# Kernel tuning notes

Hardware: AMD Instinct MI355X
Metric: run time of the kernel (lower is better)

## Reference

```python
import jax, jax.numpy as jnp
import numpy as np

NUM_NODES = 50000

def _gat_conv(x, edge_index, W, a_src, a_dst, b):
    # PyG GATConv, heads=1: h = x W ; e_ij = LeakyReLU(a_src.h_j + a_dst.h_i)
    # softmax over incoming edges of i ; out_i = sum_j alpha_ij h_j + b
    h = x @ W                                  # [N, F]
    src, dst = edge_index[0], edge_index[1]    # edge j->i : src=j, dst=i
    alpha_s = h @ a_src                        # [N]
    alpha_d = h @ a_dst                        # [N]
    e = jax.nn.leaky_relu(alpha_s[src] + alpha_d[dst], negative_slope=0.2)  # [E]
    # segment softmax over destination nodes
    e_max = jax.ops.segment_max(e, dst, num_segments=NUM_NODES)
    e_exp = jnp.exp(e - e_max[dst])
    denom = jax.ops.segment_sum(e_exp, dst, num_segments=NUM_NODES)
    coef = e_exp / denom[dst]                  # [E]
    out = jax.ops.segment_sum(h[src] * coef[:, None], dst, num_segments=NUM_NODES)
    return out + b

def setup_inputs() -> dict:
    key = jax.random.key(0)
    ks = jax.random.split(key, 10)
    N, E, IN, HID, OUT = NUM_NODES, 800000, 256, 256, 128
    x = jax.random.normal(ks[0], (N, IN), dtype=jnp.float32)
    edge_index = jax.random.randint(ks[1], (2, E), 0, N, dtype=jnp.int32)
    def glorot(k, shape):
        lim = float(np.sqrt(6.0 / (shape[0] + shape[-1])))
        return jax.random.uniform(k, shape, jnp.float32, -lim, lim)
    return {
        'x': x,
        'edge_index': edge_index,
        'W1': glorot(ks[2], (IN, HID)),
        'a_src1': glorot(ks[3], (HID,)),
        'a_dst1': glorot(ks[4], (HID,)),
        'b1': jnp.zeros((HID,), jnp.float32),
        'W2': glorot(ks[5], (HID, OUT)),
        'a_src2': glorot(ks[6], (OUT,)),
        'a_dst2': glorot(ks[7], (OUT,)),
        'b2': jnp.zeros((OUT,), jnp.float32),
    }

def reference(x, edge_index, W1, a_src1, a_dst1, b1, W2, a_src2, a_dst2, b2):
    # add self loops once (same edge_index used by both convs)
    ar = jnp.arange(NUM_NODES, dtype=edge_index.dtype)
    ei = jnp.concatenate([edge_index, jnp.stack([ar, ar])], axis=1)
    x1 = _gat_conv(x, ei, W1, a_src1, a_dst1, b1)
    h = jax.nn.relu(x1)          # dropout p=0.3 is identity in eval mode
    x2 = _gat_conv(h, ei, W2, a_src2, a_dst2, b2)
    return (x2, h)
```

## Files before the change

kernel.cpp:

```cpp
#include <hip/hip_runtime.h>
#include <hip/hip_bf16.h>

#define N_NODES 50000
#define E0      800000
#define ETOT    850000

typedef __bf16 bf16x8 __attribute__((ext_vector_type(8)));
typedef float  f32x4  __attribute__((ext_vector_type(4)));
typedef ushort u16x8  __attribute__((ext_vector_type(8)));
union B8 { u16x8 u; bf16x8 b; };

static __device__ __forceinline__ float b2f(ushort u) {
    union { uint u; float f; } x; x.u = ((uint)u) << 16; return x.f;
}
static __device__ __forceinline__ ushort f2bf(float f) {
    uint u = __builtin_bit_cast(uint, f);
    uint r = (u + 0x7FFFu + ((u >> 16) & 1u)) >> 16;
    return (ushort)r;
}


__global__ __launch_bounds__(256) void k_deg(const int* __restrict__ ei, int* __restrict__ deg) {
    int e = blockIdx.x * 256 + threadIdx.x;
    if (e >= ETOT) return;
    int dst = (e < E0) ? ei[E0 + e] : (e - E0);
    atomicAdd(&deg[dst], 1);
}

__global__ __launch_bounds__(256) void k_scan1(const int* __restrict__ deg, int* __restrict__ offs,
                                               int* __restrict__ bsum) {
    __shared__ int buf[256];
    int tid = threadIdx.x;
    int i = blockIdx.x * 256 + tid;
    int v = (i < N_NODES) ? deg[i] : 0;
    buf[tid] = v;
    __syncthreads();
    for (int off = 1; off < 256; off <<= 1) {
        int t = (tid >= off) ? buf[tid - off] : 0;
        __syncthreads();
        buf[tid] += t;
        __syncthreads();
    }
    if (i < N_NODES) offs[i + 1] = buf[tid];
    if (tid == 255) bsum[blockIdx.x] = buf[255];
}

__global__ __launch_bounds__(256) void k_scan2(int* __restrict__ bsum, int nb) {
    __shared__ int buf[256];
    int tid = threadIdx.x;
    int v = (tid < nb) ? bsum[tid] : 0;
    buf[tid] = v;
    __syncthreads();
    for (int off = 1; off < 256; off <<= 1) {
        int t = (tid >= off) ? buf[tid - off] : 0;
        __syncthreads();
        buf[tid] += t;
        __syncthreads();
    }
    if (tid < nb) bsum[tid] = buf[tid] - v;
}

__global__ __launch_bounds__(256) void k_scan3(int* __restrict__ offs, const int* __restrict__ bsum) {
    int tid = threadIdx.x;
    int i = blockIdx.x * 256 + tid;
    if (i < N_NODES) offs[i + 1] += bsum[blockIdx.x];
    if (i == 0) offs[0] = 0;
}

__global__ __launch_bounds__(256) void k_copy(const int* __restrict__ offs, int* __restrict__ cursor) {
    int i = blockIdx.x * 256 + threadIdx.x;
    if (i < N_NODES) cursor[i] = offs[i];
}

__global__ __launch_bounds__(256) void k_scatter(const int* __restrict__ ei, int* __restrict__ cursor,
                                                 int* __restrict__ esrc) {
    int e = blockIdx.x * 256 + threadIdx.x;
    if (e >= ETOT) return;
    int src, dst;
    if (e < E0) { src = ei[e]; dst = ei[E0 + e]; }
    else        { src = e - E0; dst = src; }
    int pos = atomicAdd(&cursor[dst], 1);
    esrc[pos] = src;
}

__global__ __launch_bounds__(256) void k_splitT(const float* __restrict__ W, ushort* __restrict__ th,
                                                ushort* __restrict__ tl, int K, int N) {
    int i = blockIdx.x * 256 + threadIdx.x;
    if (i >= K * N) return;
    int n = i / K, k = i - n * K;
    float v = W[(size_t)k * N + n];
    ushort h = f2bf(v);
    th[(size_t)n * K + k] = h;
    tl[(size_t)n * K + k] = f2bf(v - b2f(h));
}


static __device__ __forceinline__ void split8r(const float4 r0, const float4 r1, bf16x8& hi, bf16x8& lo) {
    float vv[8] = { r0.x, r0.y, r0.z, r0.w, r1.x, r1.y, r1.z, r1.w };
    B8 H, L;
#pragma unroll
    for (int i = 0; i < 8; ++i) {
        uint u = __builtin_bit_cast(uint, vv[i]);
        H.u[i] = (ushort)(u >> 16);
        float hf = __builtin_bit_cast(float, u & 0xffff0000u);
        L.u[i] = (ushort)(__builtin_bit_cast(uint, vv[i] - hf) >> 16);
    }
    hi = H.b; lo = L.b;
}

__global__ __launch_bounds__(256) void k_gemm_mfma(const float* __restrict__ A,
                                                   const ushort* __restrict__ Bth, const ushort* __restrict__ Btl,
                                                   ushort* __restrict__ Cb, int M, int Nn) {
    constexpr int K = 256;
    int tid = threadIdx.x;
    int wid = tid >> 6, lane = tid & 63;
    int wr = wid >> 1, wc = wid & 1;
    int bm = blockIdx.x * 128, bn = blockIdx.y * 128;
    int lr = lane & 15, lg = lane >> 4;

    f32x4 acc[4][4] = {};

    const float* Ap[4];
#pragma unroll
    for (int m = 0; m < 4; ++m) {
        int row = bm + wr * 64 + m * 16 + lr;
        if (row >= M) row = M - 1;
        Ap[m] = A + (size_t)row * K + lg * 8;
    }
    const ushort* Bhp[4];
    const ushort* Blp[4];
#pragma unroll
    for (int n = 0; n < 4; ++n) {
        int col = bn + wc * 64 + n * 16 + lr;
        Bhp[n] = Bth + (size_t)col * K + lg * 8;
        Blp[n] = Btl + (size_t)col * K + lg * 8;
    }

    float4 aR[2][4][2];
    bf16x8 bH[2][4], bL[2][4];
#pragma unroll
    for (int m = 0; m < 4; ++m) {
        aR[0][m][0] = *(const float4*)(Ap[m]);
        aR[0][m][1] = *(const float4*)(Ap[m] + 4);
    }
#pragma unroll
    for (int n = 0; n < 4; ++n) {
        bH[0][n] = *(const bf16x8*)(Bhp[n]);
        bL[0][n] = *(const bf16x8*)(Blp[n]);
    }

#pragma unroll
    for (int it = 0; it < 8; ++it) {
        const int cur = it & 1, nxt = cur ^ 1;
        if (it < 7) {
            const int kt = (it + 1) * 32;
#pragma unroll
            for (int m = 0; m < 4; ++m) {
                aR[nxt][m][0] = *(const float4*)(Ap[m] + kt);
                aR[nxt][m][1] = *(const float4*)(Ap[m] + kt + 4);
            }
#pragma unroll
            for (int n = 0; n < 4; ++n) {
                bH[nxt][n] = *(const bf16x8*)(Bhp[n] + kt);
                bL[nxt][n] = *(const bf16x8*)(Blp[n] + kt);
            }
        }
        bf16x8 a_h[4], a_l[4];
#pragma unroll
        for (int m = 0; m < 4; ++m) split8r(aR[cur][m][0], aR[cur][m][1], a_h[m], a_l[m]);
#pragma unroll
        for (int m = 0; m < 4; ++m)
#pragma unroll
            for (int n = 0; n < 4; ++n) {
                acc[m][n] = __builtin_amdgcn_mfma_f32_16x16x32_bf16(a_h[m], bH[cur][n], acc[m][n], 0, 0, 0);
                acc[m][n] = __builtin_amdgcn_mfma_f32_16x16x32_bf16(a_l[m], bH[cur][n], acc[m][n], 0, 0, 0);
                acc[m][n] = __builtin_amdgcn_mfma_f32_16x16x32_bf16(a_h[m], bL[cur][n], acc[m][n], 0, 0, 0);
            }
    }
#pragma unroll
    for (int m = 0; m < 4; ++m)
#pragma unroll
        for (int r = 0; r < 4; ++r) {
            int row = bm + wr * 64 + m * 16 + lg * 4 + r;
            if (row < M) {
#pragma unroll
                for (int n = 0; n < 4; ++n) {
                    int col = bn + wc * 64 + n * 16 + lr;
                    Cb[(size_t)row * Nn + col] = f2bf(acc[m][n][r]);
                }
            }
        }
}


template <int F>
__global__ __launch_bounds__(256) void k_alpha(const ushort* __restrict__ H, const float* __restrict__ a_src,
                                               const float* __restrict__ a_dst, float* __restrict__ as,
                                               float* __restrict__ ad) {
    int gw = (blockIdx.x * 256 + threadIdx.x) >> 6;
    int lane = threadIdx.x & 63;
    if (gw >= N_NODES) return;
    float s = 0.f, d = 0.f;
    if (F == 256) {
        ushort4 v = *(const ushort4*)(H + (size_t)gw * 256 + lane * 4);
        float4 cs = *(const float4*)(a_src + lane * 4);
        float4 cd = *(const float4*)(a_dst + lane * 4);
        float f0 = b2f(v.x), f1 = b2f(v.y), f2 = b2f(v.z), f3 = b2f(v.w);
        s = f0 * cs.x + f1 * cs.y + f2 * cs.z + f3 * cs.w;
        d = f0 * cd.x + f1 * cd.y + f2 * cd.z + f3 * cd.w;
    } else {
        ushort2 v = *(const ushort2*)(H + (size_t)gw * 128 + lane * 2);
        float2 cs = *(const float2*)(a_src + lane * 2);
        float2 cd = *(const float2*)(a_dst + lane * 2);
        float f0 = b2f(v.x), f1 = b2f(v.y);
        s = f0 * cs.x + f1 * cs.y;
        d = f0 * cd.x + f1 * cd.y;
    }
    for (int o = 32; o; o >>= 1) { s += __shfl_down(s, o); d += __shfl_down(d, o); }
    if (lane == 0) { as[gw] = s; ad[gw] = d; }
}

template <int F, bool RELU>
__global__ __launch_bounds__(256) void k_aggf(const int* __restrict__ offs, const int* __restrict__ esrc,
                                              const float* __restrict__ as, const float* __restrict__ ad,
                                              const ushort* __restrict__ H, const float* __restrict__ bias,
                                              float* __restrict__ out) {
    constexpr int V = F / 64;
    constexpr float THR = 8.f;
    int gw = (blockIdx.x * 256 + threadIdx.x) >> 6;
    int lane = threadIdx.x & 63;
    if (gw >= N_NODES) return;
    int s0 = offs[gw], s1 = offs[gw + 1];
    float adi = ad[gw];
    float m = -1e30f, ssum = 0.f;
    float acc[V] = {};
    int k = s0;
    for (; k + 3 < s1; k += 4) {
        int r0 = esrc[k], r1 = esrc[k + 1], r2 = esrc[k + 2], r3 = esrc[k + 3];
        float row0[V], row1[V], row2[V], row3[V];
        if (V == 4) {
            ushort4 v0 = *(const ushort4*)(H + (size_t)r0 * F + lane * 4);
            ushort4 v1 = *(const ushort4*)(H + (size_t)r1 * F + lane * 4);
            ushort4 v2 = *(const ushort4*)(H + (size_t)r2 * F + lane * 4);
            ushort4 v3 = *(const ushort4*)(H + (size_t)r3 * F + lane * 4);
            row0[0] = b2f(v0.x); row0[1] = b2f(v0.y); row0[2] = b2f(v0.z); row0[3] = b2f(v0.w);
            row1[0] = b2f(v1.x); row1[1] = b2f(v1.y); row1[2] = b2f(v1.z); row1[3] = b2f(v1.w);
            row2[0] = b2f(v2.x); row2[1] = b2f(v2.y); row2[2] = b2f(v2.z); row2[3] = b2f(v2.w);
            row3[0] = b2f(v3.x); row3[1] = b2f(v3.y); row3[2] = b2f(v3.z); row3[3] = b2f(v3.w);
        } else {
            ushort2 v0 = *(const ushort2*)(H + (size_t)r0 * F + lane * 2);
            ushort2 v1 = *(const ushort2*)(H + (size_t)r1 * F + lane * 2);
            ushort2 v2 = *(const ushort2*)(H + (size_t)r2 * F + lane * 2);
            ushort2 v3 = *(const ushort2*)(H + (size_t)r3 * F + lane * 2);
            row0[0] = b2f(v0.x); row0[1] = b2f(v0.y);
            row1[0] = b2f(v1.x); row1[1] = b2f(v1.y);
            row2[0] = b2f(v2.x); row2[1] = b2f(v2.y);
            row3[0] = b2f(v3.x); row3[1] = b2f(v3.y);
        }
        float e0 = as[r0] + adi; e0 = e0 > 0.f ? e0 : 0.2f * e0;
        float e1 = as[r1] + adi; e1 = e1 > 0.f ? e1 : 0.2f * e1;
        float e2 = as[r2] + adi; e2 = e2 > 0.f ? e2 : 0.2f * e2;
        float e3 = as[r3] + adi; e3 = e3 > 0.f ? e3 : 0.2f * e3;
        float em = fmaxf(fmaxf(e0, e1), fmaxf(e2, e3));
        if (em > m + THR) {
            float sc = __expf(m - em);
            ssum *= sc;
#pragma unroll
            for (int j = 0; j < V; ++j) acc[j] *= sc;
            m = em;
        }
        float w0 = __expf(e0 - m), w1 = __expf(e1 - m);
        float w2 = __expf(e2 - m), w3 = __expf(e3 - m);
        ssum += (w0 + w1) + (w2 + w3);
#pragma unroll
        for (int j = 0; j < V; ++j)
            acc[j] += (w0 * row0[j] + w1 * row1[j]) + (w2 * row2[j] + w3 * row3[j]);
    }
    for (; k < s1; ++k) {
        int r0 = esrc[k];
        float row0[V];
        if (V == 4) {
            ushort4 v0 = *(const ushort4*)(H + (size_t)r0 * F + lane * 4);
            row0[0] = b2f(v0.x); row0[1] = b2f(v0.y); row0[2] = b2f(v0.z); row0[3] = b2f(v0.w);
        } else {
            ushort2 v0 = *(const ushort2*)(H + (size_t)r0 * F + lane * 2);
            row0[0] = b2f(v0.x); row0[1] = b2f(v0.y);
        }
        float e0 = as[r0] + adi; e0 = e0 > 0.f ? e0 : 0.2f * e0;
        if (e0 > m + THR) {
            float sc = __expf(m - e0);
            ssum *= sc;
#pragma unroll
            for (int j = 0; j < V; ++j) acc[j] *= sc;
            m = e0;
        }
        float w0 = __expf(e0 - m);
        ssum += w0;
#pragma unroll
        for (int j = 0; j < V; ++j) acc[j] += w0 * row0[j];
    }
    float inv = 1.f / ssum;
    float r[V];
#pragma unroll
    for (int j = 0; j < V; ++j) {
        r[j] = acc[j] * inv + bias[lane * V + j];
        if (RELU) r[j] = fmaxf(r[j], 0.f);
    }
    if (V == 4) *(float4*)(out + (size_t)gw * F + lane * 4) = make_float4(r[0], r[1], r[2], r[3]);
    else        *(float2*)(out + (size_t)gw * F + lane * 2) = make_float2(r[0], r[1]);
}


static inline size_t al256(size_t x) { return (x + 255) & ~(size_t)255; }

extern "C" void kernel_launch(void* const* d_in, const int* in_sizes, int n_in,
                              void* d_out, int out_size, void* d_ws, size_t ws_size,
                              hipStream_t stream) {
    const float* x   = (const float*)d_in[0];
    const int*   ei  = (const int*)d_in[1];
    const float* W1  = (const float*)d_in[2];
    const float* as1 = (const float*)d_in[3];
    const float* ad1 = (const float*)d_in[4];
    const float* b1  = (const float*)d_in[5];
    const float* W2  = (const float*)d_in[6];
    const float* as2 = (const float*)d_in[7];
    const float* ad2 = (const float*)d_in[8];
    const float* b2  = (const float*)d_in[9];

    float* out_x2 = (float*)d_out;
    float* out_h  = (float*)d_out + (size_t)N_NODES * 128;

    const size_t NM256 = (size_t)N_NODES * 256 * 2;
    char* base = (char*)d_ws;
    size_t off = 0;
    auto take = [&](size_t bytes) { char* p = base + off; off = al256(off + bytes); return p; };

    ushort* h1b  = (ushort*)take(NM256);
    ushort* w1th = (ushort*)take(256 * 256 * 2);
    ushort* w1tl = (ushort*)take(256 * 256 * 2);
    ushort* w2th = (ushort*)take(256 * 128 * 2);
    ushort* w2tl = (ushort*)take(256 * 128 * 2);
    float*  asb  = (float*)take(N_NODES * 4);
    float*  adb  = (float*)take(N_NODES * 4);
    int*    deg  = (int*)take(N_NODES * 4);
    int*    offs = (int*)take((N_NODES + 4) * 4);
    int*    curs = (int*)take(N_NODES * 4);
    int*    bsum = (int*)take(1024);
    int*    esrc = (int*)take((size_t)ETOT * 4);
    (void)ws_size;

    hipMemsetAsync(deg, 0, N_NODES * sizeof(int), stream);

    int nbE = (ETOT + 255) / 256;
    int nbN = (N_NODES + 255) / 256;
    int nbW = (N_NODES * 64 + 255) / 256;

    k_deg<<<nbE, 256, 0, stream>>>(ei, deg);
    k_scan1<<<nbN, 256, 0, stream>>>(deg, offs, bsum);
    k_scan2<<<1, 256, 0, stream>>>(bsum, nbN);
    k_scan3<<<nbN, 256, 0, stream>>>(offs, bsum);
    k_copy<<<nbN, 256, 0, stream>>>(offs, curs);
    k_scatter<<<nbE, 256, 0, stream>>>(ei, curs, esrc);

    k_splitT<<<(256 * 256 + 255) / 256, 256, 0, stream>>>(W1, w1th, w1tl, 256, 256);
    k_splitT<<<(256 * 128 + 255) / 256, 256, 0, stream>>>(W2, w2th, w2tl, 256, 128);

    dim3 g1((N_NODES + 127) / 128, 2), g2((N_NODES + 127) / 128, 1);

    k_gemm_mfma<<<g1, 256, 0, stream>>>(x, w1th, w1tl, h1b, N_NODES, 256);
    k_alpha<256><<<nbW, 256, 0, stream>>>(h1b, as1, ad1, asb, adb);
    k_aggf<256, true><<<nbW, 256, 0, stream>>>(offs, esrc, asb, adb, h1b, b1, out_h);

    ushort* gb = h1b;
    k_gemm_mfma<<<g2, 256, 0, stream>>>(out_h, w2th, w2tl, gb, N_NODES, 128);
    k_alpha<128><<<nbW, 256, 0, stream>>>(gb, as2, ad2, asb, adb);
    k_aggf<128, false><<<nbW, 256, 0, stream>>>(offs, esrc, asb, adb, gb, b2, out_x2);
}
```

Measured before the change: 329.9 us.

## Stage GEMM B tiles through double-buffered LDS and fuse cursor copy into scan

The GEMM now loads the transposed hi/lo bf16 weight tiles cooperatively into a double-buffered shared-memory array, 64 K at a time. Before, each wave read B fragments straight from global memory, and waves in the same block loaded duplicate data. A-operand prefetch is reorganized to run two K-steps ahead, and launch bounds request 2 blocks per CU. Separately, the k_copy kernel is removed by having k_scan3 write the cursor array at the same time, which saves one launch. The LDS staging adds barriers and costs 64KB of shared memory per block, which may limit occupancy.

```diff
diff --git a/kernel.cpp b/kernel.cpp
--- a/kernel.cpp
+++ b/kernel.cpp
@@ -60,16 +60,16 @@
     if (tid < nb) bsum[tid] = buf[tid] - v;
 }
 
-__global__ __launch_bounds__(256) void k_scan3(int* __restrict__ offs, const int* __restrict__ bsum) {
+__global__ __launch_bounds__(256) void k_scan3(int* __restrict__ offs, const int* __restrict__ bsum,
+                                               int* __restrict__ cursor) {
     int tid = threadIdx.x;
     int i = blockIdx.x * 256 + tid;
-    if (i < N_NODES) offs[i + 1] += bsum[blockIdx.x];
-    if (i == 0) offs[0] = 0;
-}
-
-__global__ __launch_bounds__(256) void k_copy(const int* __restrict__ offs, int* __restrict__ cursor) {
-    int i = blockIdx.x * 256 + threadIdx.x;
-    if (i < N_NODES) cursor[i] = offs[i];
+    if (i < N_NODES) {
+        int v = offs[i + 1] + bsum[blockIdx.x];
+        offs[i + 1] = v;
+        cursor[i + 1] = v;
+    }
+    if (i == 0) { offs[0] = 0; cursor[0] = 0; }
 }
 
 __global__ __launch_bounds__(256) void k_scatter(const int* __restrict__ ei, int* __restrict__ cursor,
@@ -108,17 +108,20 @@
     hi = H.b; lo = L.b;
 }
 
-__global__ __launch_bounds__(256) void k_gemm_mfma(const float* __restrict__ A,
-                                                   const ushort* __restrict__ Bth, const ushort* __restrict__ Btl,
-                                                   ushort* __restrict__ Cb, int M, int Nn) {
+__global__ __launch_bounds__(256, 2) void k_gemm_mfma(const float* __restrict__ A,
+                                                      const ushort* __restrict__ Bth,
+                                                      const ushort* __restrict__ Btl,
+                                                      ushort* __restrict__ Cb, int M, int Nn) {
     constexpr int K = 256;
+    __shared__ ushort lds[2][2][8][128][8];
     int tid = threadIdx.x;
     int wid = tid >> 6, lane = tid & 63;
     int wr = wid >> 1, wc = wid & 1;
     int bm = blockIdx.x * 128, bn = blockIdx.y * 128;
     int lr = lane & 15, lg = lane >> 4;
 
-    f32x4 acc[4][4] = {};
+    int sa = tid >> 7, scol = tid & 127;
+    const ushort* sb = (sa ? Btl : Bth) + (size_t)(bn + scol) * K;
 
     const float* Ap[4];
 #pragma unroll
@@ -127,55 +130,63 @@
         if (row >= M) row = M - 1;
         Ap[m] = A + (size_t)row * K + lg * 8;
     }
-    const ushort* Bhp[4];
-    const ushort* Blp[4];
-#pragma unroll
-    for (int n = 0; n < 4; ++n) {
-        int col = bn + wc * 64 + n * 16 + lr;
-        Bhp[n] = Bth + (size_t)col * K + lg * 8;
-        Blp[n] = Btl + (size_t)col * K + lg * 8;
-    }
-
+
+    f32x4 acc[4][4] = {};
+    u16x8 sv[8];
     float4 aR[2][4][2];
-    bf16x8 bH[2][4], bL[2][4];
+
+#pragma unroll
+    for (int c = 0; c < 8; ++c) sv[c] = *(const u16x8*)(sb + c * 8);
 #pragma unroll
     for (int m = 0; m < 4; ++m) {
         aR[0][m][0] = *(const float4*)(Ap[m]);
         aR[0][m][1] = *(const float4*)(Ap[m] + 4);
-    }
-#pragma unroll
-    for (int n = 0; n < 4; ++n) {
-        bH[0][n] = *(const bf16x8*)(Bhp[n]);
-        bL[0][n] = *(const bf16x8*)(Blp[n]);
-    }
-
-#pragma unroll
-    for (int it = 0; it < 8; ++it) {
-        const int cur = it & 1, nxt = cur ^ 1;
-        if (it < 7) {
-            const int kt = (it + 1) * 32;
+        aR[1][m][0] = *(const float4*)(Ap[m] + 32);
+        aR[1][m][1] = *(const float4*)(Ap[m] + 36);
+    }
+#pragma unroll
+    for (int c = 0; c < 8; ++c) *(u16x8*)&lds[0][sa][c][scol][0] = sv[c];
+    __syncthreads();
+
+#pragma unroll
+    for (int s = 0; s < 8; ++s) {
+        const int w = s >> 1, buf = w & 1, kk = s & 1;
+        if (kk == 0 && w < 3) {
+#pragma unroll
+            for (int c = 0; c < 8; ++c) sv[c] = *(const u16x8*)(sb + (w + 1) * 64 + c * 8);
+        }
+        bf16x8 bh[4], bl[4];
+#pragma unroll
+        for (int n = 0; n < 4; ++n) {
+            int col = wc * 64 + n * 16 + lr;
+            B8 th, tl2;
+            th.u = *(const u16x8*)&lds[buf][0][kk * 4 + lg][col][0];
+            tl2.u = *(const u16x8*)&lds[buf][1][kk * 4 + lg][col][0];
+            bh[n] = th.b; bl[n] = tl2.b;
+        }
+        bf16x8 ah[4], al[4];
+#pragma unroll
+        for (int m = 0; m < 4; ++m) split8r(aR[s & 1][m][0], aR[s & 1][m][1], ah[m], al[m]);
+        if (s < 6) {
 #pragma unroll
             for (int m = 0; m < 4; ++m) {
-                aR[nxt][m][0] = *(const float4*)(Ap[m] + kt);
-                aR[nxt][m][1] = *(const float4*)(Ap[m] + kt + 4);
+                aR[s & 1][m][0] = *(const float4*)(Ap[m] + (s + 2) * 32);
+                aR[s & 1][m][1] = *(const float4*)(Ap[m] + (s + 2) * 32 + 4);
             }
+        }
+#pragma unroll
+        for (int m = 0; m < 4; ++m)
 #pragma unroll
             for (int n = 0; n < 4; ++n) {
-                bH[nxt][n] = *(const bf16x8*)(Bhp[n] + kt);
-                bL[nxt][n] = *(const bf16x8*)(Blp[n] + kt);
+                acc[m][n] = __builtin_amdgcn_mfma_f32_16x16x32_bf16(ah[m], bh[n], acc[m][n], 0, 0, 0);
+                acc[m][n] = __builtin_amdgcn_mfma_f32_16x16x32_bf16(al[m], bh[n], acc[m][n], 0, 0, 0);
+                acc[m][n] = __builtin_amdgcn_mfma_f32_16x16x32_bf16(ah[m], bl[n], acc[m][n], 0, 0, 0);
             }
-        }
-        bf16x8 a_h[4], a_l[4];
-#pragma unroll
-        for (int m = 0; m < 4; ++m) split8r(aR[cur][m][0], aR[cur][m][1], a_h[m], a_l[m]);
-#pragma unroll
-        for (int m = 0; m < 4; ++m)
-#pragma unroll
-            for (int n = 0; n < 4; ++n) {
-                acc[m][n] = __builtin_amdgcn_mfma_f32_16x16x32_bf16(a_h[m], bH[cur][n], acc[m][n], 0, 0, 0);
-                acc[m][n] = __builtin_amdgcn_mfma_f32_16x16x32_bf16(a_l[m], bH[cur][n], acc[m][n], 0, 0, 0);
-                acc[m][n] = __builtin_amdgcn_mfma_f32_16x16x32_bf16(a_h[m], bL[cur][n], acc[m][n], 0, 0, 0);
-            }
+        if (kk == 1 && w < 3) {
+#pragma unroll
+            for (int c = 0; c < 8; ++c) *(u16x8*)&lds[buf ^ 1][sa][c][scol][0] = sv[c];
+            __syncthreads();
+        }
     }
 #pragma unroll
     for (int m = 0; m < 4; ++m)
@@ -344,7 +355,7 @@
     float*  adb  = (float*)take(N_NODES * 4);
     int*    deg  = (int*)take(N_NODES * 4);
     int*    offs = (int*)take((N_NODES + 4) * 4);
-    int*    curs = (int*)take(N_NODES * 4);
+    int*    curs = (int*)take((N_NODES + 4) * 4);
     int*    bsum = (int*)take(1024);
     int*    esrc = (int*)take((size_t)ETOT * 4);
     (void)ws_size;
@@ -358,8 +369,7 @@
     k_deg<<<nbE, 256, 0, stream>>>(ei, deg);
     k_scan1<<<nbN, 256, 0, stream>>>(deg, offs, bsum);
     k_scan2<<<1, 256, 0, stream>>>(bsum, nbN);
-    k_scan3<<<nbN, 256, 0, stream>>>(offs, bsum);
-    k_copy<<<nbN, 256, 0, stream>>>(offs, curs);
+    k_scan3<<<nbN, 256, 0, stream>>>(offs, bsum, curs);
     k_scatter<<<nbE, 256, 0, stream>>>(ei, curs, esrc);
 
     k_splitT<<<(256 * 256 + 255) / 256, 256, 0, stream>>>(W1, w1th, w1tl, 256, 256);
```

Measured after the change: 310.2 us. -6.0%, faster.
